# Optimization experiments

Measured on AMD Instinct MI355X. Metric: run time of the kernel, lower is better.

The kernel has to match this reference:

```python
import jax, jax.numpy as jnp
import numpy as np

EPS = 1e-8


def _conv1(x, w):
    # x: [C,H,W], w: [O,C,k,k] -> [O,H,W] (SAME padding, stride 1)
    return jax.lax.conv_general_dilated(
        x[None], w, window_strides=(1, 1), padding='SAME',
        dimension_numbers=('NCHW', 'OIHW', 'NCHW'))[0]


def setup_inputs() -> dict:
    key = jax.random.key(0)
    k1, k2, k3, k4 = jax.random.split(key, 4)
    B, C, O, K, S, H, W = 8, 512, 512, 3, 512, 64, 64
    inp = jax.random.normal(k1, (B, C, H, W), dtype=jnp.float32)
    style = jax.random.normal(k2, (B, S), dtype=jnp.float32)
    weight = jax.random.normal(k3, (1, O, C, K, K), dtype=jnp.float32)  # conv weight
    mod_weight = jax.random.normal(k4, (C, S), dtype=jnp.float32)      # EqualLinear weight
    mod_bias = jnp.ones((C,), dtype=jnp.float32)                        # bias filled with 1.0
    return {"input": inp, "style": style, "weight": weight,
            "mod_weight": mod_weight, "mod_bias": mod_bias}


def reference(input, style, weight, mod_weight, mod_bias) -> jnp.ndarray:
    B, C, H, W = input.shape
    _, O, _, K, _ = weight.shape
    fan_in = C * K * K
    scale = 1.0 / np.sqrt(fan_in)
    lin_scale = 1.0 / np.sqrt(mod_weight.shape[1])

    # EqualLinear modulation: [B, C]
    s = style @ (mod_weight * lin_scale).T + mod_bias

    # Modulate + demodulate per-sample weights: [B, O, C, K, K]
    w = scale * weight * s[:, None, :, None, None]
    demod = jax.lax.rsqrt(jnp.sum(w * w, axis=(2, 3, 4)) + EPS)  # [B, O]
    w = w * demod[:, :, None, None, None]

    # Grouped conv with groups=B == per-sample conv, vmapped over batch
    out = jax.vmap(_conv1)(input, w)  # [B, O, H, W]
    return out
```

## Files before the change

### kernel.cpp

```cpp
#include <hip/hip_runtime.h>

typedef unsigned short u16;
typedef __bf16 bf16_t;
typedef bf16_t bf16x8 __attribute__((ext_vector_type(8)));
typedef float floatx4 __attribute__((ext_vector_type(4)));

static constexpr float kScale = 0.014731391274719741f;
static constexpr float kScale2 = 2.1701388888888894e-4f;
static constexpr float kLinScale = 0.044194173824159216f;

__device__ __forceinline__ u16 f2bf(float f) {
  unsigned u = __float_as_uint(f);
  u += 0x7FFFu + ((u >> 16) & 1u);
  return (u16)(u >> 16);
}

#define GLD16(g, l)                                                        \
  __builtin_amdgcn_global_load_lds(                                        \
      (const __attribute__((address_space(1))) unsigned int*)(g),          \
      (__attribute__((address_space(3))) unsigned int*)(l), 16, 0, 0)

__global__ __launch_bounds__(256) void k_prep1(const float* __restrict__ style,
                                               const float* __restrict__ modw,
                                               const float* __restrict__ modb,
                                               const float* __restrict__ weight,
                                               float* __restrict__ s_buf,
                                               float* __restrict__ ssq) {
  int tid = threadIdx.x;
  if (blockIdx.x < 1024) {
    int lane = tid & 63, wv = tid >> 6;
    int idx = blockIdx.x * 4 + wv;
    int b = idx >> 9, c = idx & 511;
    const float* st = style + b * 512;
    const float* mw = modw + (size_t)c * 512;
    float s = 0.f;
#pragma unroll
    for (int i = 0; i < 8; ++i) s += st[lane + i * 64] * mw[lane + i * 64];
#pragma unroll
    for (int off = 32; off; off >>= 1) s += __shfl_xor(s, off);
    if (lane == 0) s_buf[idx] = s * kLinScale + modb[c];
  } else {
    int e = (blockIdx.x - 1024) * 256 + tid;
    const float* wp = weight + (size_t)e * 9;
    float ss = 0.f;
#pragma unroll
    for (int t = 0; t < 9; ++t) ss += wp[t] * wp[t];
    ssq[e] = ss;
  }
}

__global__ __launch_bounds__(256) void k_fused2(const float* __restrict__ in,
                                                const float* __restrict__ s_buf,
                                                const float* __restrict__ weight,
                                                const float* __restrict__ ssq,
                                                unsigned* __restrict__ in_t32,
                                                unsigned* __restrict__ wt32,
                                                float* __restrict__ demod_buf) {
  __shared__ char shm[9216];
  int tid = threadIdx.x;
  int bid = blockIdx.x;
  if (bid < 4096) {
    u16* tile = (u16*)shm;
    int c0 = (bid & 7) * 64, y = (bid >> 3) & 63, b = bid >> 9;
    const float* src = in + ((size_t)(b * 512 + c0) * 4096) + y * 64;
    const float* srow = s_buf + b * 512 + c0;
#pragma unroll
    for (int it = 0; it < 16; ++it) {
      int idx = it * 256 + tid;
      int cl = idx >> 6, x = idx & 63;
      tile[cl * 65 + x] = f2bf(src[(size_t)cl * 4096 + x] * srow[cl]);
    }
    __syncthreads();
    unsigned* dst = in_t32 + ((size_t)(b * 64 + y) * 64) * 256 + (c0 >> 1);
#pragma unroll
    for (int it = 0; it < 8; ++it) {
      int flat = it * 256 + tid;
      int cl2 = flat & 31, x = flat >> 5;
      unsigned lo = tile[(2 * cl2) * 65 + x];
      unsigned hi = tile[(2 * cl2 + 1) * 65 + x];
      dst[(size_t)x * 256 + cl2] = lo | (hi << 16);
    }
  } else if (bid < 4608) {
    u16(*tiles)[512] = (u16(*)[512])shm;
    int w = bid - 4096;
    int ct = w & 15, ot = w >> 4;
    int o0 = ot * 16, c0 = ct * 32;
#pragma unroll
    for (int i = 0; i < 18; ++i) {
      int flat = i * 256 + tid;
      int t9 = flat / 9;
      int tap = flat - t9 * 9;
      int o_l = t9 >> 5, c_l = t9 & 31;
      float wt = weight[((size_t)(o0 + o_l) * 512 + c0 + c_l) * 9 + tap];
      int pos = ((o_l + ((c_l >> 3) << 4)) << 3) + (c_l & 7);
      tiles[tap][pos] = f2bf(wt * kScale);
    }
    __syncthreads();
    const unsigned* tl = (const unsigned*)tiles;
#pragma unroll
    for (int tap = 0; tap < 9; ++tap)
      wt32[(size_t)((tap * 16 + ct) * 32 + ot) * 256 + tid] = tl[tap * 256 + tid];
  } else {
    int lane = tid & 63, wv = tid >> 6;
    int idx = (bid - 4608) * 4 + wv;
    int b = idx >> 9, o = idx & 511;
    const float* sq = ssq + (size_t)o * 512;
    const float* srow = s_buf + b * 512;
    float ss = 0.f;
#pragma unroll
    for (int i = 0; i < 8; ++i) {
      float s = srow[lane + i * 64];
      ss += sq[lane + i * 64] * s * s;
    }
#pragma unroll
    for (int off = 32; off; off >>= 1) ss += __shfl_xor(ss, off);
    if (lane == 0) demod_buf[idx] = rsqrtf(ss * kScale2 + 1e-8f);
  }
}

__global__ __launch_bounds__(256, 2) void k_conv(const u16* __restrict__ in_t,
                                                 const u16* __restrict__ w_t,
                                                 const float* __restrict__ demod_buf,
                                                 float* __restrict__ out) {
  __shared__ char smem[67584];
  const int tid = threadIdx.x;
  const int lane = tid & 63;
  const int wv = tid >> 6;
  const int wm = wv >> 1, wn = wv & 1;
  const int quad = lane >> 4, m16 = lane & 15;
  const int lin = blockIdx.x + 32 * blockIdx.y + 128 * blockIdx.z;
  const int b = lin & 7;
  const int r_ = lin >> 3;
  const int nt = r_ & 31;
  const int mt = r_ >> 5;
  const int y0 = nt * 2;

  floatx4 acc[4][4];
#pragma unroll
  for (int i = 0; i < 4; ++i)
#pragma unroll
    for (int j = 0; j < 4; ++j) acc[i][j] = (floatx4){0.f, 0.f, 0.f, 0.f};

  const u16* abase = w_t + mt * 4096 + wm * 2048 + lane * 8;

  const int xs = tid >> 3, qs = tid & 7;
  const int cch = qs ^ (xs & 7);
  const u16* gB[4];
  bool rok[4];
#pragma unroll
  for (int r = 0; r < 4; ++r) {
    int y = y0 - 1 + r;
    rok[r] = (unsigned)y < 64u;
    gB[r] = in_t + (((size_t)(b * 64 + (rok[r] ? y : 0)) * 64 + xs) * 512 + cch * 8);
  }

  char* bA[6];
#pragma unroll
  for (int dx = 0; dx < 3; ++dx) {
    const int sx0 = m16 + dx - 1;
#pragma unroll
    for (int kh = 0; kh < 2; ++kh)
      bA[dx * 2 + kh] = smem + wn * 8448 + (sx0 + 1) * 128 +
                        (((kh * 4 + quad) ^ (sx0 & 7)) << 4);
  }

  bf16x8 aR[2][2][4];
  bf16x8 bv[2][2][4];

#define LOAD_BV(si, bufimm, t_)                                              \
  {                                                                          \
    const int dy_ = (t_) / 3, dx_ = (t_) % 3;                                \
    _Pragma("unroll") for (int kh = 0; kh < 2; ++kh)                         \
      _Pragma("unroll") for (int ns = 0; ns < 4; ++ns)                       \
        bv[si][kh][ns] = *(const bf16x8*)(bA[dx_ * 2 + kh] + (bufimm) +      \
                                          dy_ * 8448 + ns * 2048);           \
  }

#define STAGE_B(bufimm)                                                      \
  {                                                                          \
    _Pragma("unroll") for (int r = 0; r < 4; ++r)                            \
      if (rok[r]) {                                                          \
        GLD16(gB[r], smem + (bufimm) + r * 8448 + 128 + wv * 1024);          \
        GLD16(gB[r] + 16384,                                                 \
              smem + (bufimm) + r * 8448 + 128 + 4096 + wv * 1024);          \
      }                                                                      \
  }

#define LOAD_A2(si, tp_, ctp_)                                               \
  {                                                                          \
    _Pragma("unroll") for (int kh = 0; kh < 2; ++kh) {                       \
      const u16* ap_ =                                                       \
          abase + ((size_t)((tp_)*16 + 2 * (ctp_) + kh) << 14);              \
      _Pragma("unroll") for (int ms = 0; ms < 4; ++ms)                       \
        aR[si][kh][ms] = *(const bf16x8*)(ap_ + ms * 512);                   \
    }                                                                        \
  }

#define CT_BODY(ctv, par, CURIMM, NXTIMM)                                    \
  {                                                                          \
    LOAD_BV(par, CURIMM, 0);                                                 \
    if ((ctv) + 1 < 8) {                                                     \
      _Pragma("unroll") for (int r = 0; r < 4; ++r) gB[r] += 64;             \
      STAGE_B(NXTIMM);                                                       \
    }                                                                        \
    _Pragma("unroll") for (int t = 0; t < 9; ++t) {                          \
      const int icur = (t + (par)) & 1;                                      \
      const int inxt = icur ^ 1;                                             \
      const int tp = t < 8 ? t + 1 : 0;                                      \
      const int ctp = t < 8 ? (ctv) : (ctv) + 1;                             \
      LOAD_A2(inxt, tp, ctp);                                                \
      if (t < 8) { LOAD_BV(inxt, CURIMM, t + 1); }                           \
      __builtin_amdgcn_s_setprio(1);                                         \
      _Pragma("unroll") for (int kh = 0; kh < 2; ++kh)                       \
        _Pragma("unroll") for (int ns = 0; ns < 4; ++ns)                     \
          _Pragma("unroll") for (int ms = 0; ms < 4; ++ms)                   \
            acc[ms][ns] = __builtin_amdgcn_mfma_f32_16x16x32_bf16(           \
                aR[icur][kh][ms], bv[icur][kh][ns], acc[ms][ns], 0, 0, 0);   \
      __builtin_amdgcn_s_setprio(0);                                         \
    }                                                                        \
    asm volatile("s_waitcnt vmcnt(8)" ::: "memory");                         \
    __builtin_amdgcn_s_barrier();                                            \
  }

  {
    const uint4 z = make_uint4(0u, 0u, 0u, 0u);
    for (int i = tid; i < 4224; i += 256) ((uint4*)smem)[i] = z;
  }
  __syncthreads();
  STAGE_B(0);
  __syncthreads();
  LOAD_A2(0, 0, 0);

  for (int ct = 0; ct < 8; ct += 2) {
    CT_BODY(ct, 0, 0, 33792);
    CT_BODY(ct + 1, 1, 33792, 0);
  }

#undef LOAD_BV
#undef STAGE_B
#undef LOAD_A2
#undef CT_BODY

  const int ob = mt * 128 + wm * 64;
  const int nb = nt * 128 + wn * 64;
#pragma unroll
  for (int ms = 0; ms < 4; ++ms)
#pragma unroll
    for (int ns = 0; ns < 4; ++ns) {
      const int n = nb + ns * 16 + m16;
#pragma unroll
      for (int r = 0; r < 4; ++r) {
        const int o = ob + ms * 16 + quad * 4 + r;
        float dm = demod_buf[b * 512 + o];
        out[((size_t)(b * 512 + o) << 12) + n] = acc[ms][ns][r] * dm;
      }
    }
}

extern "C" void kernel_launch(void* const* d_in, const int* in_sizes, int n_in,
                              void* d_out, int out_size, void* d_ws, size_t ws_size,
                              hipStream_t stream) {
  const float* input = (const float*)d_in[0];
  const float* style = (const float*)d_in[1];
  const float* weight = (const float*)d_in[2];
  const float* modw = (const float*)d_in[3];
  const float* modb = (const float*)d_in[4];
  float* out = (float*)d_out;
  char* ws = (char*)d_ws;
  float* s_buf = (float*)ws;
  float* demod_buf = (float*)(ws + 16384);
  float* ssq = (float*)(ws + 32768);
  u16* in_t = (u16*)(ws + 32768 + 1048576);
  u16* w_t = (u16*)(ws + 32768 + 1048576 + 33554432);

  k_prep1<<<dim3(2048), dim3(256), 0, stream>>>(style, modw, modb, weight, s_buf, ssq);
  k_fused2<<<dim3(5632), dim3(256), 0, stream>>>(input, s_buf, weight, ssq,
                                                 (unsigned*)in_t, (unsigned*)w_t,
                                                 demod_buf);
  k_conv<<<dim3(32, 4, 8), dim3(256), 0, stream>>>(in_t, w_t, demod_buf, out);
}
```

Measured before the change: 242.4 us.

## Vectorize input transpose-prep loads/stores and remap conv block-to-tile ordering

The input modulation and transpose stage now reads float4 vectors and writes ushort4 values into a tile whose rows are padded to 68. The transposed data is then emitted as 16-byte uint4 stores instead of scalar 32-bit writes, which cuts the number of global memory instructions. The conv kernel's linear block index is also remapped so consecutive blocks cover different output-channel tiles and batches for the same spatial tile. This is meant to change which weight and input data are shared among concurrently running blocks, improving cache reuse. The padding of 68 may add LDS bank conflicts in the strided reads of the transpose.

```diff
diff --git a/kernel.cpp b/kernel.cpp
--- a/kernel.cpp
+++ b/kernel.cpp
@@ -65,20 +65,31 @@
     const float* src = in + ((size_t)(b * 512 + c0) * 4096) + y * 64;
     const float* srow = s_buf + b * 512 + c0;
 #pragma unroll
-    for (int it = 0; it < 16; ++it) {
+    for (int it = 0; it < 4; ++it) {
       int idx = it * 256 + tid;
-      int cl = idx >> 6, x = idx & 63;
-      tile[cl * 65 + x] = f2bf(src[(size_t)cl * 4096 + x] * srow[cl]);
+      int cl = idx >> 4, xq = idx & 15;
+      float4 v = *(const float4*)(src + (size_t)cl * 4096 + xq * 4);
+      float s = srow[cl];
+      ushort4 o;
+      o.x = f2bf(v.x * s);
+      o.y = f2bf(v.y * s);
+      o.z = f2bf(v.z * s);
+      o.w = f2bf(v.w * s);
+      *(ushort4*)(&tile[cl * 68 + xq * 4]) = o;
     }
     __syncthreads();
     unsigned* dst = in_t32 + ((size_t)(b * 64 + y) * 64) * 256 + (c0 >> 1);
 #pragma unroll
-    for (int it = 0; it < 8; ++it) {
-      int flat = it * 256 + tid;
-      int cl2 = flat & 31, x = flat >> 5;
-      unsigned lo = tile[(2 * cl2) * 65 + x];
-      unsigned hi = tile[(2 * cl2 + 1) * 65 + x];
-      dst[(size_t)x * 256 + cl2] = lo | (hi << 16);
+    for (int it = 0; it < 2; ++it) {
+      int idx = it * 256 + tid;
+      int cg = idx & 7, x = idx >> 3;
+      const u16* tb = &tile[cg * 8 * 68 + x];
+      uint4 w;
+      w.x = tb[0 * 68] | ((unsigned)tb[1 * 68] << 16);
+      w.y = tb[2 * 68] | ((unsigned)tb[3 * 68] << 16);
+      w.z = tb[4 * 68] | ((unsigned)tb[5 * 68] << 16);
+      w.w = tb[6 * 68] | ((unsigned)tb[7 * 68] << 16);
+      *(uint4*)(dst + (size_t)x * 256 + cg * 4) = w;
     }
   } else if (bid < 4608) {
     u16(*tiles)[512] = (u16(*)[512])shm;
@@ -129,10 +140,12 @@
   const int wm = wv >> 1, wn = wv & 1;
   const int quad = lane >> 4, m16 = lane & 15;
   const int lin = blockIdx.x + 32 * blockIdx.y + 128 * blockIdx.z;
-  const int b = lin & 7;
+  const int low = lin & 7;
+  const int mt = low >> 1;
+  const int p = low & 1;
   const int r_ = lin >> 3;
-  const int nt = r_ & 31;
-  const int mt = r_ >> 5;
+  const int b = ((r_ & 3) << 1) | p;
+  const int nt = r_ >> 2;
   const int y0 = nt * 2;
 
   floatx4 acc[4][4];
```

Result: slower. 249.7 us (+3.0%).
